# Kernel tuning notes

Hardware: AMD Instinct MI355X
Metric: run time of the kernel (lower is better)

## Reference

```python
import jax, jax.numpy as jnp
import numpy as np

N_NODES = 100000
N_EDGES = 1600000
D_IN = 128
D_OUT = 128


def setup_inputs() -> dict:
    key = jax.random.key(0)
    k1, k2, k3 = jax.random.split(key, 3)
    x = jax.random.normal(k1, (N_NODES, D_IN), dtype=jnp.float32)
    edge_index = jax.random.randint(k2, (2, N_EDGES), 0, N_NODES, dtype=jnp.int64)
    # Xavier-uniform-like init for weight (matches nn.init.xavier_uniform_ scale)
    limit = float(np.sqrt(6.0 / (D_IN + D_OUT)))
    weight = jax.random.uniform(k3, (D_IN, D_OUT), dtype=jnp.float32,
                                minval=-limit, maxval=limit)
    bias = jnp.zeros((D_OUT,), dtype=jnp.float32)
    return {"x": x, "edge_index": edge_index, "weight": weight, "bias": bias}


def reference(x, edge_index, weight, bias):
    num_nodes = x.shape[0]
    src = edge_index[0]  # edge_index_i: gather side
    dst = edge_index[1]  # edge_index_j: scatter side

    # Degree of each node counted over src endpoints.
    deg = jax.ops.segment_sum(jnp.ones_like(src, dtype=x.dtype), src,
                              num_segments=num_nodes)
    # deg^{-1/2} with inf -> 0 for isolated nodes.
    deg_safe = jnp.where(deg > 0, deg, jnp.ones_like(deg))
    deg_inv_sqrt = jnp.where(deg > 0, jax.lax.rsqrt(deg_safe), jnp.zeros_like(deg))

    norm = deg_inv_sqrt[src] * deg_inv_sqrt[dst]  # [E]

    h = x @ weight  # [N, D_OUT]
    # Edge-parallel gather, scale, scatter-add.
    msgs = norm[:, None] * h[src]  # [E, D_OUT]
    out = jax.ops.segment_sum(msgs, dst, num_segments=num_nodes)  # [N, D_OUT]
    return out + bias
```

## Files before the change

kernel.cpp:

```cpp
#include <hip/hip_runtime.h>

#define D 128
#define CAP 64
#define STRIP_LOG 15
#define STRIP (1 << STRIP_LOG)
#define WORDS_LOG (STRIP_LOG - 2)
#define WORDS (1 << WORDS_LOG)
#define NCHUNK 128
#define LDW 136
#define LDO 132

typedef __attribute__((ext_vector_type(8))) short bf16x8;
typedef __attribute__((ext_vector_type(4))) float f32x4;

__device__ __forceinline__ unsigned f2bf(float f) {
    unsigned u = __float_as_uint(f);
    return (u + 0x7fffu + ((u >> 16) & 1u)) >> 16;
}

__device__ __forceinline__ int chunk_size(int n_edges) {
    return (((n_edges + NCHUNK - 1) / NCHUNK) + 3) & ~3;
}

__global__ __launch_bounds__(256) void k_histA(const int* __restrict__ src,
                                               const int* __restrict__ dst,
                                               unsigned* __restrict__ pb_s,
                                               unsigned* __restrict__ pb_d, int n_edges) {
    int strip = blockIdx.x / NCHUNK, chunk = blockIdx.x % NCHUNK;
    int lo = strip << STRIP_LOG;
    __shared__ unsigned hs[WORDS];
    __shared__ unsigned hd[WORDS];
    for (int i = threadIdx.x; i < WORDS; i += 256) { hs[i] = 0; hd[i] = 0; }
    __syncthreads();

    int csz = chunk_size(n_edges);
    int beg = chunk * csz;
    int end = min(beg + csz, n_edges);
    if (beg < end) {
        int aend = beg + ((end - beg) & ~3);
        for (int i = beg + threadIdx.x * 4; i + 3 < aend; i += 1024) {
            int4 s = *(const int4*)(src + i);
            int4 d = *(const int4*)(dst + i);
            unsigned b;
            b = (unsigned)(s.x - lo); if (b < STRIP) atomicAdd(&hs[b >> 2], 1u << ((b & 3) * 8));
            b = (unsigned)(s.y - lo); if (b < STRIP) atomicAdd(&hs[b >> 2], 1u << ((b & 3) * 8));
            b = (unsigned)(s.z - lo); if (b < STRIP) atomicAdd(&hs[b >> 2], 1u << ((b & 3) * 8));
            b = (unsigned)(s.w - lo); if (b < STRIP) atomicAdd(&hs[b >> 2], 1u << ((b & 3) * 8));
            b = (unsigned)(d.x - lo); if (b < STRIP) atomicAdd(&hd[b >> 2], 1u << ((b & 3) * 8));
            b = (unsigned)(d.y - lo); if (b < STRIP) atomicAdd(&hd[b >> 2], 1u << ((b & 3) * 8));
            b = (unsigned)(d.z - lo); if (b < STRIP) atomicAdd(&hd[b >> 2], 1u << ((b & 3) * 8));
            b = (unsigned)(d.w - lo); if (b < STRIP) atomicAdd(&hd[b >> 2], 1u << ((b & 3) * 8));
        }
        for (int e = aend + threadIdx.x; e < end; e += 256) {
            unsigned bs = (unsigned)(src[e] - lo);
            if (bs < STRIP) atomicAdd(&hs[bs >> 2], 1u << ((bs & 3) * 8));
            unsigned bd = (unsigned)(dst[e] - lo);
            if (bd < STRIP) atomicAdd(&hd[bd >> 2], 1u << ((bd & 3) * 8));
        }
    }
    __syncthreads();
    unsigned* ps = pb_s + (size_t)blockIdx.x * WORDS;
    unsigned* pd = pb_d + (size_t)blockIdx.x * WORDS;
    for (int i = threadIdx.x; i < WORDS; i += 256) { ps[i] = hs[i]; pd[i] = hd[i]; }
}

__global__ __launch_bounds__(256) void k_base_dis(unsigned* __restrict__ pb_d,
                                                  const unsigned* __restrict__ pb_s,
                                                  int* __restrict__ deg_dst,
                                                  float* __restrict__ dis,
                                                  int n, int nwords) {
    int gw = blockIdx.x * 256 + threadIdx.x;
    if (gw >= nwords) return;
    int strip = gw >> WORDS_LOG, widx = gw & (WORDS - 1);
    size_t base = (size_t)strip * NCHUNK * WORDS + widx;

    unsigned run[4] = {0, 0, 0, 0};
    for (int c = 0; c < NCHUNK; ++c) {
        size_t idx = base + (size_t)c * WORDS;
        unsigned v = pb_d[idx];
        pb_d[idx] = run[0] | (run[1] << 8) | (run[2] << 16) | (run[3] << 24);
        run[0] += v & 0xffu;
        run[1] += (v >> 8) & 0xffu;
        run[2] += (v >> 16) & 0xffu;
        run[3] += (v >> 24) & 0xffu;
    }
    int g0 = (strip << STRIP_LOG) + widx * 4;
    if (g0 >= n) return;

    unsigned ss[4] = {0, 0, 0, 0};
    for (int c = 0; c < NCHUNK; ++c) {
        unsigned v = pb_s[base + (size_t)c * WORDS];
        ss[0] += v & 0xffu;
        ss[1] += (v >> 8) & 0xffu;
        ss[2] += (v >> 16) & 0xffu;
        ss[3] += (v >> 24) & 0xffu;
    }
    if (g0 + 3 < n) {
        *(int4*)(deg_dst + g0) = make_int4(run[0], run[1], run[2], run[3]);
        *(float4*)(dis + g0) = make_float4(
            ss[0] ? rsqrtf((float)ss[0]) : 0.0f, ss[1] ? rsqrtf((float)ss[1]) : 0.0f,
            ss[2] ? rsqrtf((float)ss[2]) : 0.0f, ss[3] ? rsqrtf((float)ss[3]) : 0.0f);
    } else {
        #pragma unroll
        for (int j = 0; j < 4; ++j)
            if (g0 + j < n) {
                deg_dst[g0 + j] = run[j];
                dis[g0 + j] = ss[j] ? rsqrtf((float)ss[j]) : 0.0f;
            }
    }
}

__global__ __launch_bounds__(256) void k_placeB(const int* __restrict__ src,
                                                const int* __restrict__ dst,
                                                const unsigned* __restrict__ pb_d,
                                                int* __restrict__ epad, int n_edges) {
    int strip = blockIdx.x / NCHUNK, chunk = blockIdx.x % NCHUNK;
    int lo = strip << STRIP_LOG;
    __shared__ unsigned cur[WORDS];
    const unsigned* cb = pb_d + (size_t)blockIdx.x * WORDS;
    for (int i = threadIdx.x; i < WORDS; i += 256) cur[i] = cb[i];
    __syncthreads();

    int csz = chunk_size(n_edges);
    int beg = chunk * csz;
    int end = min(beg + csz, n_edges);
    if (beg < end) {
        int aend = beg + ((end - beg) & ~3);
        for (int i = beg + threadIdx.x * 4; i + 3 < aend; i += 1024) {
            int4 s = *(const int4*)(src + i);
            int4 d = *(const int4*)(dst + i);
            unsigned b, o, r;
            b = (unsigned)(d.x - lo);
            if (b < STRIP) {
                o = atomicAdd(&cur[b >> 2], 1u << ((b & 3) * 8));
                r = (o >> ((b & 3) * 8)) & 0xffu;
                if (r < CAP) epad[(((unsigned)lo + b) << 6) + r] = s.x;
            }
            b = (unsigned)(d.y - lo);
            if (b < STRIP) {
                o = atomicAdd(&cur[b >> 2], 1u << ((b & 3) * 8));
                r = (o >> ((b & 3) * 8)) & 0xffu;
                if (r < CAP) epad[(((unsigned)lo + b) << 6) + r] = s.y;
            }
            b = (unsigned)(d.z - lo);
            if (b < STRIP) {
                o = atomicAdd(&cur[b >> 2], 1u << ((b & 3) * 8));
                r = (o >> ((b & 3) * 8)) & 0xffu;
                if (r < CAP) epad[(((unsigned)lo + b) << 6) + r] = s.z;
            }
            b = (unsigned)(d.w - lo);
            if (b < STRIP) {
                o = atomicAdd(&cur[b >> 2], 1u << ((b & 3) * 8));
                r = (o >> ((b & 3) * 8)) & 0xffu;
                if (r < CAP) epad[(((unsigned)lo + b) << 6) + r] = s.w;
            }
        }
        for (int e = aend + threadIdx.x; e < end; e += 256) {
            unsigned b = (unsigned)(dst[e] - lo);
            if (b < STRIP) {
                unsigned o = atomicAdd(&cur[b >> 2], 1u << ((b & 3) * 8));
                unsigned r = (o >> ((b & 3) * 8)) & 0xffu;
                if (r < CAP) epad[(((unsigned)lo + b) << 6) + r] = src[e];
            }
        }
    }
}

__global__ __launch_bounds__(256) void k_gemm(const float* __restrict__ x,
                                              const float* __restrict__ w,
                                              const float* __restrict__ dis,
                                              unsigned* __restrict__ hb, int nrows) {
    __shared__ __align__(16) unsigned short wt[128][LDW];
    __shared__ __align__(16) float sOut[4][16][LDO];
    int tid = threadIdx.x;

    {
        const float4* w4 = (const float4*)w;
        #pragma unroll
        for (int it = 0; it < 16; ++it) {
            int i = tid + it * 256;
            int k = i >> 5, n0 = (i & 31) * 4;
            float4 v = w4[i];
            wt[n0 + 0][k] = (unsigned short)f2bf(v.x);
            wt[n0 + 1][k] = (unsigned short)f2bf(v.y);
            wt[n0 + 2][k] = (unsigned short)f2bf(v.z);
            wt[n0 + 3][k] = (unsigned short)f2bf(v.w);
        }
    }
    __syncthreads();

    int lane = tid & 63, wv = tid >> 6;
    int m = lane & 15, quad = lane >> 4;
    int rbase = blockIdx.x * 128 + wv * 32;

    int r0 = rbase + m, r1 = rbase + 16 + m;
    const float* pa0 = x + (size_t)(r0 < nrows ? r0 : 0) * D;
    const float* pa1 = x + (size_t)(r1 < nrows ? r1 : 0) * D;

    f32x4 acc[2][8] = {};
    #pragma unroll
    for (int kt = 0; kt < 4; ++kt) {
        int k0 = kt * 32 + quad * 8;
        float4 a0l = *(const float4*)(pa0 + k0);
        float4 a0h = *(const float4*)(pa0 + k0 + 4);
        float4 a1l = *(const float4*)(pa1 + k0);
        float4 a1h = *(const float4*)(pa1 + k0 + 4);
        bf16x8 a0, a1;
        a0[0] = (short)f2bf(a0l.x); a0[1] = (short)f2bf(a0l.y);
        a0[2] = (short)f2bf(a0l.z); a0[3] = (short)f2bf(a0l.w);
        a0[4] = (short)f2bf(a0h.x); a0[5] = (short)f2bf(a0h.y);
        a0[6] = (short)f2bf(a0h.z); a0[7] = (short)f2bf(a0h.w);
        a1[0] = (short)f2bf(a1l.x); a1[1] = (short)f2bf(a1l.y);
        a1[2] = (short)f2bf(a1l.z); a1[3] = (short)f2bf(a1l.w);
        a1[4] = (short)f2bf(a1h.x); a1[5] = (short)f2bf(a1h.y);
        a1[6] = (short)f2bf(a1h.z); a1[7] = (short)f2bf(a1h.w);
        bf16x8 b[8];
        #pragma unroll
        for (int ct = 0; ct < 8; ++ct)
            b[ct] = *(const bf16x8*)&wt[ct * 16 + m][k0];
        #pragma unroll
        for (int ct = 0; ct < 8; ++ct) {
            acc[0][ct] = __builtin_amdgcn_mfma_f32_16x16x32_bf16(a0, b[ct], acc[0][ct], 0, 0, 0);
            acc[1][ct] = __builtin_amdgcn_mfma_f32_16x16x32_bf16(a1, b[ct], acc[1][ct], 0, 0, 0);
        }
    }

    float* so = &sOut[wv][0][0];
    int ri = lane >> 2, qc = lane & 3;
    #pragma unroll
    for (int rt = 0; rt < 2; ++rt) {
        #pragma unroll
        for (int ct = 0; ct < 8; ++ct)
            #pragma unroll
            for (int reg = 0; reg < 4; ++reg)
                so[(quad * 4 + reg) * LDO + ct * 16 + m] = acc[rt][ct][reg];
        int row = rbase + rt * 16 + ri;
        if (row < nrows) {
            float dn = dis[row];
            const float* sr = so + ri * LDO + qc * 32;
            unsigned* hrow = hb + (size_t)row * 64 + qc * 16;
            #pragma unroll
            for (int j = 0; j < 4; ++j) {
                float2 p0 = *(const float2*)(sr + j * 8 + 0);
                float2 p1 = *(const float2*)(sr + j * 8 + 2);
                float2 p2 = *(const float2*)(sr + j * 8 + 4);
                float2 p3 = *(const float2*)(sr + j * 8 + 6);
                uint4 o;
                o.x = f2bf(dn * p0.x) | (f2bf(dn * p0.y) << 16);
                o.y = f2bf(dn * p1.x) | (f2bf(dn * p1.y) << 16);
                o.z = f2bf(dn * p2.x) | (f2bf(dn * p2.y) << 16);
                o.w = f2bf(dn * p3.x) | (f2bf(dn * p3.y) << 16);
                *(uint4*)(hrow + j * 4) = o;
            }
        }
        __builtin_amdgcn_s_waitcnt(0);
    }
}

#define ACC8(u) do { \
    ax[0] += __uint_as_float((u).x << 16); ax[1] += __uint_as_float((u).x & 0xffff0000u); \
    ax[2] += __uint_as_float((u).y << 16); ax[3] += __uint_as_float((u).y & 0xffff0000u); \
    ax[4] += __uint_as_float((u).z << 16); ax[5] += __uint_as_float((u).z & 0xffff0000u); \
    ax[6] += __uint_as_float((u).w << 16); ax[7] += __uint_as_float((u).w & 0xffff0000u); } while (0)

__global__ __launch_bounds__(256) void k_accum(const int* __restrict__ epad,
                                               const int* __restrict__ degd,
                                               const uint4* __restrict__ hb4,
                                               const float* __restrict__ dis,
                                               const float* __restrict__ bias,
                                               float* __restrict__ out, int n) {
    int wid = threadIdx.x >> 6, lane = threadIdx.x & 63;
    int node = blockIdx.x * 4 + wid;
    if (node >= n) return;
    int deg = min(degd[node], CAP);
    int g = lane >> 4, c = lane & 15;
    const int* ep = epad + (size_t)node * CAP;

    float ax[8] = {0.f, 0.f, 0.f, 0.f, 0.f, 0.f, 0.f, 0.f};
    int e = g;
    for (; e + 12 < deg; e += 16) {
        int s0 = ep[e];
        int s1 = ep[e + 4];
        int s2 = ep[e + 8];
        int s3 = ep[e + 12];
        uint4 u0 = hb4[(size_t)s0 * 16 + c];
        uint4 u1 = hb4[(size_t)s1 * 16 + c];
        uint4 u2 = hb4[(size_t)s2 * 16 + c];
        uint4 u3 = hb4[(size_t)s3 * 16 + c];
        ACC8(u0); ACC8(u1); ACC8(u2); ACC8(u3);
    }
    for (; e < deg; e += 4) {
        int s0 = ep[e];
        uint4 u0 = hb4[(size_t)s0 * 16 + c];
        ACC8(u0);
    }

    #pragma unroll
    for (int k = 0; k < 8; ++k) {
        ax[k] += __shfl_xor(ax[k], 16, 64);
        ax[k] += __shfl_xor(ax[k], 32, 64);
    }

    if (g == 0) {
        float dn = dis[node];
        float4 b0 = ((const float4*)bias)[c * 2];
        float4 b1 = ((const float4*)bias)[c * 2 + 1];
        float4 o0 = make_float4(fmaf(dn, ax[0], b0.x), fmaf(dn, ax[1], b0.y),
                                fmaf(dn, ax[2], b0.z), fmaf(dn, ax[3], b0.w));
        float4 o1 = make_float4(fmaf(dn, ax[4], b1.x), fmaf(dn, ax[5], b1.y),
                                fmaf(dn, ax[6], b1.z), fmaf(dn, ax[7], b1.w));
        float4* op = (float4*)(out + (size_t)node * D) + c * 2;
        op[0] = o0;
        op[1] = o1;
    }
}

extern "C" void kernel_launch(void* const* d_in, const int* in_sizes, int n_in,
                              void* d_out, int out_size, void* d_ws, size_t ws_size,
                              hipStream_t stream) {
    const float* x    = (const float*)d_in[0];
    const int*   ei   = (const int*)d_in[1];
    const float* w    = (const float*)d_in[2];
    const float* bias = (const float*)d_in[3];
    float* out = (float*)d_out;

    int n_edges = in_sizes[1] / 2;
    int n_nodes = in_sizes[0] / D;
    const int* src = ei;
    const int* dst = ei + n_edges;

    int nstrips = (n_nodes + STRIP - 1) >> STRIP_LOG;
    int nwords = nstrips * WORDS;

    char* ws = (char*)d_ws;
    unsigned* hb = (unsigned*)ws;      ws += (size_t)n_nodes * 64 * sizeof(unsigned);
    int* epad    = (int*)ws;           ws += (size_t)n_nodes * CAP * sizeof(int);
    int* deg_dst = (int*)ws;           ws += (size_t)n_nodes * sizeof(int);
    float* dis   = (float*)ws;         ws += (size_t)n_nodes * sizeof(float);
    unsigned* pb_s = (unsigned*)ws;    ws += (size_t)nstrips * NCHUNK * WORDS * sizeof(unsigned);
    unsigned* pb_d = (unsigned*)ws;

    k_histA<<<nstrips * NCHUNK, 256, 0, stream>>>(src, dst, pb_s, pb_d, n_edges);
    k_base_dis<<<(nwords + 255) / 256, 256, 0, stream>>>(pb_d, pb_s, deg_dst, dis,
                                                         n_nodes, nwords);
    k_gemm<<<(n_nodes + 127) / 128, 256, 0, stream>>>(x, w, dis, hb, n_nodes);
    k_placeB<<<nstrips * NCHUNK, 256, 0, stream>>>(src, dst, pb_d, epad, n_edges);
    k_accum<<<(n_nodes + 3) / 4, 256, 0, stream>>>(epad, deg_dst, (const uint4*)hb,
                                                   dis, bias, out, n_nodes);
}
```

Measured before the change: 252.1 us.

## Replace strip-partitioned histograms with whole-range LDS histograms per chunk

Histogram and placement kernels now hold the whole node range (up to 25088 packed words, about 100 KB of LDS) in one block instead of splitting nodes into 32K strips. The old version had every strip re-read all edges. Src and dst histograms now go to separate blocks by role, and the scan kernel splits dst prefix and src degree work across different threads with 8-wide unrolled loads. The cost is far fewer blocks (256 for the histogram, 128 for placement) with large LDS footprints, so occupancy is one block per CU. There is also no guard if n_nodes exceeds MAXW*4.

Result: faster. 237.7 us (median of 2 runs) (-5.7%).

```diff
diff --git a/kernel.cpp b/kernel.cpp
--- a/kernel.cpp
+++ b/kernel.cpp
@@ -2,11 +2,8 @@
 
 #define D 128
 #define CAP 64
-#define STRIP_LOG 15
-#define STRIP (1 << STRIP_LOG)
-#define WORDS_LOG (STRIP_LOG - 2)
-#define WORDS (1 << WORDS_LOG)
 #define NCHUNK 128
+#define MAXW 25088
 #define LDW 136
 #define LDO 132
 
@@ -22,15 +19,18 @@
     return (((n_edges + NCHUNK - 1) / NCHUNK) + 3) & ~3;
 }
 
-__global__ __launch_bounds__(256) void k_histA(const int* __restrict__ src,
-                                               const int* __restrict__ dst,
-                                               unsigned* __restrict__ pb_s,
-                                               unsigned* __restrict__ pb_d, int n_edges) {
-    int strip = blockIdx.x / NCHUNK, chunk = blockIdx.x % NCHUNK;
-    int lo = strip << STRIP_LOG;
-    __shared__ unsigned hs[WORDS];
-    __shared__ unsigned hd[WORDS];
-    for (int i = threadIdx.x; i < WORDS; i += 256) { hs[i] = 0; hd[i] = 0; }
+__global__ __launch_bounds__(512) void k_hist(const int* __restrict__ src,
+                                              const int* __restrict__ dst,
+                                              unsigned* __restrict__ pb_s,
+                                              unsigned* __restrict__ pb_d,
+                                              int n_edges, int wtot) {
+    __shared__ unsigned h[MAXW];
+    int chunk = blockIdx.x % NCHUNK;
+    int role  = blockIdx.x / NCHUNK;
+    const int* ids = role ? src : dst;
+    unsigned* pb   = role ? pb_s : pb_d;
+    int tid = threadIdx.x;
+    for (int i = tid; i < wtot; i += 512) h[i] = 0;
     __syncthreads();
 
     int csz = chunk_size(n_edges);
@@ -38,87 +38,93 @@
     int end = min(beg + csz, n_edges);
     if (beg < end) {
         int aend = beg + ((end - beg) & ~3);
-        for (int i = beg + threadIdx.x * 4; i + 3 < aend; i += 1024) {
-            int4 s = *(const int4*)(src + i);
-            int4 d = *(const int4*)(dst + i);
+        for (int i = beg + tid * 4; i + 3 < aend; i += 2048) {
+            int4 v = *(const int4*)(ids + i);
             unsigned b;
-            b = (unsigned)(s.x - lo); if (b < STRIP) atomicAdd(&hs[b >> 2], 1u << ((b & 3) * 8));
-            b = (unsigned)(s.y - lo); if (b < STRIP) atomicAdd(&hs[b >> 2], 1u << ((b & 3) * 8));
-            b = (unsigned)(s.z - lo); if (b < STRIP) atomicAdd(&hs[b >> 2], 1u << ((b & 3) * 8));
-            b = (unsigned)(s.w - lo); if (b < STRIP) atomicAdd(&hs[b >> 2], 1u << ((b & 3) * 8));
-            b = (unsigned)(d.x - lo); if (b < STRIP) atomicAdd(&hd[b >> 2], 1u << ((b & 3) * 8));
-            b = (unsigned)(d.y - lo); if (b < STRIP) atomicAdd(&hd[b >> 2], 1u << ((b & 3) * 8));
-            b = (unsigned)(d.z - lo); if (b < STRIP) atomicAdd(&hd[b >> 2], 1u << ((b & 3) * 8));
-            b = (unsigned)(d.w - lo); if (b < STRIP) atomicAdd(&hd[b >> 2], 1u << ((b & 3) * 8));
-        }
-        for (int e = aend + threadIdx.x; e < end; e += 256) {
-            unsigned bs = (unsigned)(src[e] - lo);
-            if (bs < STRIP) atomicAdd(&hs[bs >> 2], 1u << ((bs & 3) * 8));
-            unsigned bd = (unsigned)(dst[e] - lo);
-            if (bd < STRIP) atomicAdd(&hd[bd >> 2], 1u << ((bd & 3) * 8));
+            b = (unsigned)v.x; atomicAdd(&h[b >> 2], 1u << ((b & 3) * 8));
+            b = (unsigned)v.y; atomicAdd(&h[b >> 2], 1u << ((b & 3) * 8));
+            b = (unsigned)v.z; atomicAdd(&h[b >> 2], 1u << ((b & 3) * 8));
+            b = (unsigned)v.w; atomicAdd(&h[b >> 2], 1u << ((b & 3) * 8));
+        }
+        for (int e = aend + tid; e < end; e += 512) {
+            unsigned b = (unsigned)ids[e];
+            atomicAdd(&h[b >> 2], 1u << ((b & 3) * 8));
         }
     }
     __syncthreads();
-    unsigned* ps = pb_s + (size_t)blockIdx.x * WORDS;
-    unsigned* pd = pb_d + (size_t)blockIdx.x * WORDS;
-    for (int i = threadIdx.x; i < WORDS; i += 256) { ps[i] = hs[i]; pd[i] = hd[i]; }
-}
-
-__global__ __launch_bounds__(256) void k_base_dis(unsigned* __restrict__ pb_d,
-                                                  const unsigned* __restrict__ pb_s,
-                                                  int* __restrict__ deg_dst,
-                                                  float* __restrict__ dis,
-                                                  int n, int nwords) {
-    int gw = blockIdx.x * 256 + threadIdx.x;
-    if (gw >= nwords) return;
-    int strip = gw >> WORDS_LOG, widx = gw & (WORDS - 1);
-    size_t base = (size_t)strip * NCHUNK * WORDS + widx;
-
-    unsigned run[4] = {0, 0, 0, 0};
-    for (int c = 0; c < NCHUNK; ++c) {
-        size_t idx = base + (size_t)c * WORDS;
-        unsigned v = pb_d[idx];
-        pb_d[idx] = run[0] | (run[1] << 8) | (run[2] << 16) | (run[3] << 24);
-        run[0] += v & 0xffu;
-        run[1] += (v >> 8) & 0xffu;
-        run[2] += (v >> 16) & 0xffu;
-        run[3] += (v >> 24) & 0xffu;
-    }
-    int g0 = (strip << STRIP_LOG) + widx * 4;
-    if (g0 >= n) return;
-
-    unsigned ss[4] = {0, 0, 0, 0};
-    for (int c = 0; c < NCHUNK; ++c) {
-        unsigned v = pb_s[base + (size_t)c * WORDS];
-        ss[0] += v & 0xffu;
-        ss[1] += (v >> 8) & 0xffu;
-        ss[2] += (v >> 16) & 0xffu;
-        ss[3] += (v >> 24) & 0xffu;
-    }
-    if (g0 + 3 < n) {
-        *(int4*)(deg_dst + g0) = make_int4(run[0], run[1], run[2], run[3]);
-        *(float4*)(dis + g0) = make_float4(
-            ss[0] ? rsqrtf((float)ss[0]) : 0.0f, ss[1] ? rsqrtf((float)ss[1]) : 0.0f,
-            ss[2] ? rsqrtf((float)ss[2]) : 0.0f, ss[3] ? rsqrtf((float)ss[3]) : 0.0f);
-    } else {
-        #pragma unroll
-        for (int j = 0; j < 4; ++j)
-            if (g0 + j < n) {
-                deg_dst[g0 + j] = run[j];
-                dis[g0 + j] = ss[j] ? rsqrtf((float)ss[j]) : 0.0f;
+    unsigned* p = pb + (size_t)chunk * wtot;
+    for (int i = tid; i < wtot; i += 512) p[i] = h[i];
+}
+
+__global__ __launch_bounds__(256) void k_scan(unsigned* __restrict__ pb_d,
+                                              const unsigned* __restrict__ pb_s,
+                                              int* __restrict__ deg_dst,
+                                              float* __restrict__ dis,
+                                              int n, int wtot) {
+    int t = blockIdx.x * 256 + threadIdx.x;
+    if (t < wtot) {
+        int w = t;
+        unsigned run[4] = {0, 0, 0, 0};
+        for (int cb = 0; cb < NCHUNK; cb += 8) {
+            unsigned v[8];
+            #pragma unroll
+            for (int j = 0; j < 8; ++j) v[j] = pb_d[(size_t)(cb + j) * wtot + w];
+            #pragma unroll
+            for (int j = 0; j < 8; ++j) {
+                pb_d[(size_t)(cb + j) * wtot + w] =
+                    run[0] | (run[1] << 8) | (run[2] << 16) | (run[3] << 24);
+                run[0] += v[j] & 0xffu;
+                run[1] += (v[j] >> 8) & 0xffu;
+                run[2] += (v[j] >> 16) & 0xffu;
+                run[3] += (v[j] >> 24) & 0xffu;
             }
-    }
-}
-
-__global__ __launch_bounds__(256) void k_placeB(const int* __restrict__ src,
-                                                const int* __restrict__ dst,
-                                                const unsigned* __restrict__ pb_d,
-                                                int* __restrict__ epad, int n_edges) {
-    int strip = blockIdx.x / NCHUNK, chunk = blockIdx.x % NCHUNK;
-    int lo = strip << STRIP_LOG;
-    __shared__ unsigned cur[WORDS];
-    const unsigned* cb = pb_d + (size_t)blockIdx.x * WORDS;
-    for (int i = threadIdx.x; i < WORDS; i += 256) cur[i] = cb[i];
+        }
+        int g0 = w * 4;
+        if (g0 + 3 < n) {
+            *(int4*)(deg_dst + g0) = make_int4(run[0], run[1], run[2], run[3]);
+        } else {
+            #pragma unroll
+            for (int j = 0; j < 4; ++j)
+                if (g0 + j < n) deg_dst[g0 + j] = run[j];
+        }
+    } else if (t < 2 * wtot) {
+        int w = t - wtot;
+        unsigned ss[4] = {0, 0, 0, 0};
+        for (int cb = 0; cb < NCHUNK; cb += 8) {
+            unsigned v[8];
+            #pragma unroll
+            for (int j = 0; j < 8; ++j) v[j] = pb_s[(size_t)(cb + j) * wtot + w];
+            #pragma unroll
+            for (int j = 0; j < 8; ++j) {
+                ss[0] += v[j] & 0xffu;
+                ss[1] += (v[j] >> 8) & 0xffu;
+                ss[2] += (v[j] >> 16) & 0xffu;
+                ss[3] += (v[j] >> 24) & 0xffu;
+            }
+        }
+        int g0 = w * 4;
+        if (g0 + 3 < n) {
+            *(float4*)(dis + g0) = make_float4(
+                ss[0] ? rsqrtf((float)ss[0]) : 0.0f, ss[1] ? rsqrtf((float)ss[1]) : 0.0f,
+                ss[2] ? rsqrtf((float)ss[2]) : 0.0f, ss[3] ? rsqrtf((float)ss[3]) : 0.0f);
+        } else {
+            #pragma unroll
+            for (int j = 0; j < 4; ++j)
+                if (g0 + j < n) dis[g0 + j] = ss[j] ? rsqrtf((float)ss[j]) : 0.0f;
+        }
+    }
+}
+
+__global__ __launch_bounds__(512) void k_place(const int* __restrict__ src,
+                                               const int* __restrict__ dst,
+                                               const unsigned* __restrict__ pb_d,
+                                               int* __restrict__ epad,
+                                               int n_edges, int wtot) {
+    __shared__ unsigned cur[MAXW];
+    int chunk = blockIdx.x;
+    int tid = threadIdx.x;
+    const unsigned* cb = pb_d + (size_t)chunk * wtot;
+    for (int i = tid; i < wtot; i += 512) cur[i] = cb[i];
     __syncthreads();
 
     int csz = chunk_size(n_edges);
@@ -126,42 +132,32 @@
     int end = min(beg + csz, n_edges);
     if (beg < end) {
         int aend = beg + ((end - beg) & ~3);
-        for (int i = beg + threadIdx.x * 4; i + 3 < aend; i += 1024) {
+        for (int i = beg + tid * 4; i + 3 < aend; i += 2048) {
             int4 s = *(const int4*)(src + i);
             int4 d = *(const int4*)(dst + i);
             unsigned b, o, r;
-            b = (unsigned)(d.x - lo);
-            if (b < STRIP) {
-                o = atomicAdd(&cur[b >> 2], 1u << ((b & 3) * 8));
-                r = (o >> ((b & 3) * 8)) & 0xffu;
-                if (r < CAP) epad[(((unsigned)lo + b) << 6) + r] = s.x;
-            }
-            b = (unsigned)(d.y - lo);
-            if (b < STRIP) {
-                o = atomicAdd(&cur[b >> 2], 1u << ((b & 3) * 8));
-                r = (o >> ((b & 3) * 8)) & 0xffu;
-                if (r < CAP) epad[(((unsigned)lo + b) << 6) + r] = s.y;
-            }
-            b = (unsigned)(d.z - lo);
-            if (b < STRIP) {
-                o = atomicAdd(&cur[b >> 2], 1u << ((b & 3) * 8));
-                r = (o >> ((b & 3) * 8)) & 0xffu;
-                if (r < CAP) epad[(((unsigned)lo + b) << 6) + r] = s.z;
-            }
-            b = (unsigned)(d.w - lo);
-            if (b < STRIP) {
-                o = atomicAdd(&cur[b >> 2], 1u << ((b & 3) * 8));
-                r = (o >> ((b & 3) * 8)) & 0xffu;
-                if (r < CAP) epad[(((unsigned)lo + b) << 6) + r] = s.w;
-            }
-        }
-        for (int e = aend + threadIdx.x; e < end; e += 256) {
-            unsigned b = (unsigned)(dst[e] - lo);
-            if (b < STRIP) {
-                unsigned o = atomicAdd(&cur[b >> 2], 1u << ((b & 3) * 8));
-                unsigned r = (o >> ((b & 3) * 8)) & 0xffu;
-                if (r < CAP) epad[(((unsigned)lo + b) << 6) + r] = src[e];
-            }
+            b = (unsigned)d.x;
+            o = atomicAdd(&cur[b >> 2], 1u << ((b & 3) * 8));
+            r = (o >> ((b & 3) * 8)) & 0xffu;
+            if (r < CAP) epad[((size_t)b << 6) + r] = s.x;
+            b = (unsigned)d.y;
+            o = atomicAdd(&cur[b >> 2], 1u << ((b & 3) * 8));
+            r = (o >> ((b & 3) * 8)) & 0xffu;
+            if (r < CAP) epad[((size_t)b << 6) + r] = s.y;
+            b = (unsigned)d.z;
+            o = atomicAdd(&cur[b >> 2], 1u << ((b & 3) * 8));
+            r = (o >> ((b & 3) * 8)) & 0xffu;
+            if (r < CAP) epad[((size_t)b << 6) + r] = s.z;
+            b = (unsigned)d.w;
+            o = atomicAdd(&cur[b >> 2], 1u << ((b & 3) * 8));
+            r = (o >> ((b & 3) * 8)) & 0xffu;
+            if (r < CAP) epad[((size_t)b << 6) + r] = s.w;
+        }
+        for (int e = aend + tid; e < end; e += 512) {
+            unsigned b = (unsigned)dst[e];
+            unsigned o = atomicAdd(&cur[b >> 2], 1u << ((b & 3) * 8));
+            unsigned r = (o >> ((b & 3) * 8)) & 0xffu;
+            if (r < CAP) epad[((size_t)b << 6) + r] = src[e];
         }
     }
 }
@@ -329,22 +325,21 @@
     const int* src = ei;
     const int* dst = ei + n_edges;
 
-    int nstrips = (n_nodes + STRIP - 1) >> STRIP_LOG;
-    int nwords = nstrips * WORDS;
+    int wtot = (n_nodes + 3) / 4;
 
     char* ws = (char*)d_ws;
     unsigned* hb = (unsigned*)ws;      ws += (size_t)n_nodes * 64 * sizeof(unsigned);
     int* epad    = (int*)ws;           ws += (size_t)n_nodes * CAP * sizeof(int);
     int* deg_dst = (int*)ws;           ws += (size_t)n_nodes * sizeof(int);
     float* dis   = (float*)ws;         ws += (size_t)n_nodes * sizeof(float);
-    unsigned* pb_s = (unsigned*)ws;    ws += (size_t)nstrips * NCHUNK * WORDS * sizeof(unsigned);
+    unsigned* pb_s = (unsigned*)ws;    ws += (size_t)NCHUNK * wtot * sizeof(unsigned);
     unsigned* pb_d = (unsigned*)ws;
 
-    k_histA<<<nstrips * NCHUNK, 256, 0, stream>>>(src, dst, pb_s, pb_d, n_edges);
-    k_base_dis<<<(nwords + 255) / 256, 256, 0, stream>>>(pb_d, pb_s, deg_dst, dis,
-                                                         n_nodes, nwords);
+    k_hist<<<2 * NCHUNK, 512, 0, stream>>>(src, dst, pb_s, pb_d, n_edges, wtot);
+    k_scan<<<(2 * wtot + 255) / 256, 256, 0, stream>>>(pb_d, pb_s, deg_dst, dis,
+                                                       n_nodes, wtot);
     k_gemm<<<(n_nodes + 127) / 128, 256, 0, stream>>>(x, w, dis, hb, n_nodes);
-    k_placeB<<<nstrips * NCHUNK, 256, 0, stream>>>(src, dst, pb_d, epad, n_edges);
+    k_place<<<NCHUNK, 512, 0, stream>>>(src, dst, pb_d, epad, n_edges, wtot);
     k_accum<<<(n_nodes + 3) / 4, 256, 0, stream>>>(epad, deg_dst, (const uint4*)hb,
                                                    dis, bias, out, n_nodes);
 }
```
